# Optimization experiments

Hardware: AMD Instinct MI355X
Metric: run time of the kernel (lower is better)

Reference implementation:

```python
import jax, jax.numpy as jnp
import numpy as np

D_MODEL = 768
N_HEADS = 12
D_K = D_MODEL // N_HEADS
NEG_INF = -1e9


def setup_inputs() -> dict:
    key = jax.random.key(0)
    ks = jax.random.split(key, 7)
    B, S = 4, 2048
    x = jax.random.normal(ks[0], (B, S, D_MODEL), dtype=jnp.float32)
    # causal mask, broadcastable to [B, H, S, S]
    mask = jnp.tril(jnp.ones((S, S), dtype=bool))[None, None, :, :]
    scale = 1.0 / np.sqrt(D_MODEL)
    Wq = jax.random.normal(ks[1], (D_MODEL, D_MODEL), dtype=jnp.float32) * scale
    bq = jnp.zeros((D_MODEL,), dtype=jnp.float32)
    Wk = jax.random.normal(ks[2], (D_MODEL, D_MODEL), dtype=jnp.float32) * scale
    bk = jnp.zeros((D_MODEL,), dtype=jnp.float32)
    Wv = jax.random.normal(ks[3], (D_MODEL, D_MODEL), dtype=jnp.float32) * scale
    bv = jnp.zeros((D_MODEL,), dtype=jnp.float32)
    return {"x": x, "mask": mask, "Wq": Wq, "bq": bq, "Wk": Wk, "bk": bk, "Wv": Wv, "bv": bv}


def reference(x, mask, Wq, bq, Wk, bk, Wv, bv):
    B, S, _ = x.shape
    # projections (torch Linear: y = x @ W.T + b)
    q = (x @ Wq.T + bq).reshape(B, S, N_HEADS, D_K)
    k = (x @ Wk.T + bk).reshape(B, S, N_HEADS, D_K)
    v = (x @ Wv.T + bv).reshape(B, S, N_HEADS, D_K)
    # scores: [B, H, S, S]
    scores = jnp.einsum("bqhd,bkhd->bhqk", q, k) / jnp.sqrt(jnp.float32(D_K))
    scores = jnp.where(mask, scores, NEG_INF)
    probs = jax.nn.softmax(scores, axis=-1)
    # attention: [B, H, S, D_K] -> [B, S, d_model]
    attn = jnp.einsum("bhqk,bkhd->bqhd", probs, v).reshape(B, S, D_MODEL)
    return attn
```

## Files before the change

kernel.cpp:

```cpp
#include <hip/hip_runtime.h>
#include <math.h>


#define S_LEN 2048
#define BATCH 4
#define HEADS 12
#define DM 768
#define DK 64
#define BH (BATCH*HEADS)
#define MROWS (BATCH*S_LEN)
#define QSCALE 0.1803368801111244f

typedef __attribute__((ext_vector_type(8))) short short8;
typedef __attribute__((ext_vector_type(4))) float floatx4;
typedef __attribute__((address_space(3))) unsigned char lds_byte;
typedef __attribute__((address_space(1))) const unsigned char glob_byte;

__device__ __forceinline__ unsigned short f2bf(float f) {
  union { float f; unsigned int u; } a; a.f = f;
  unsigned int u = a.u;
  return (unsigned short)((u + 0x7fffu + ((u >> 16) & 1u)) >> 16);
}
__device__ __forceinline__ unsigned short f2bf_rtz(float f) {
  union { float f; unsigned int u; } a; a.f = f;
  return (unsigned short)(a.u >> 16);
}

__global__ void cast_f32_bf16(const float* __restrict__ src,
                              unsigned short* __restrict__ dst, int n) {
  int i = (blockIdx.x * blockDim.x + threadIdx.x) * 4;
  if (i < n) {
    float4 v = *(const float4*)(src + i);
    ushort4 o;
    o.x = f2bf(v.x); o.y = f2bf(v.y); o.z = f2bf(v.z); o.w = f2bf(v.w);
    *(ushort4*)(dst + i) = o;
  }
}

__global__ void cast_w3(const float* __restrict__ w0, const float* __restrict__ w1,
                        const float* __restrict__ w2, unsigned short* __restrict__ dst,
                        int n) {
  const float* src = (blockIdx.y == 0) ? w0 : (blockIdx.y == 1) ? w1 : w2;
  int i = (blockIdx.x * blockDim.x + threadIdx.x) * 4;
  if (i < n) {
    float4 v = *(const float4*)(src + i);
    ushort4 o;
    o.x = f2bf(v.x); o.y = f2bf(v.y); o.z = f2bf(v.z); o.w = f2bf(v.w);
    *(ushort4*)(dst + (size_t)blockIdx.y * n + i) = o;
  }
}

__global__ __launch_bounds__(256) void qkv_gemm(
    const unsigned short* __restrict__ xb,
    const unsigned short* __restrict__ wb,
    const float* __restrict__ bq, const float* __restrict__ bk,
    const float* __restrict__ bv,
    unsigned short* __restrict__ qo,
    unsigned short* __restrict__ ko,
    unsigned short* __restrict__ vto) {
  __shared__ unsigned short a_lds[2 * 128 * 32];
  __shared__ unsigned short b_lds[2 * 128 * 32];
  const int mat = blockIdx.z;
  const int tid = threadIdx.x;
  const int wave = tid >> 6, lane = tid & 63, quad = lane >> 4, ln = lane & 15;
  const int wm = wave & 1, wn = wave >> 1;
  const int m_blk = blockIdx.x * 128, n_blk = blockIdx.y * 128;
  const unsigned short* w = wb + (size_t)mat * DM * DM;
  const int srow_i[2] = { (0 * 256 + wave * 64 + lane) >> 2,
                          (1 * 256 + wave * 64 + lane) >> 2 };
  const int sq = (lane & 3) * 8;

  const floatx4 fz = {0.f, 0.f, 0.f, 0.f};
  floatx4 acc[4][4];
#pragma unroll
  for (int mg = 0; mg < 4; mg++)
#pragma unroll
    for (int c = 0; c < 4; c++) acc[mg][c] = fz;

  for (int k0 = 0; k0 < DM; k0 += 64) {
#pragma unroll
    for (int p = 0; p < 2; p++)
#pragma unroll
      for (int i = 0; i < 2; i++) {
        const int cbase = i * 256 + wave * 64;
        const int row = srow_i[i];
        __builtin_amdgcn_global_load_lds(
            (glob_byte*)(xb + (size_t)(m_blk + row) * DM + k0 + p * 32 + sq),
            (lds_byte*)(a_lds + p * 4096 + cbase * 8), 16, 0, 0);
        __builtin_amdgcn_global_load_lds(
            (glob_byte*)(w + (size_t)(n_blk + row) * DM + k0 + p * 32 + sq),
            (lds_byte*)(b_lds + p * 4096 + cbase * 8), 16, 0, 0);
      }
    __syncthreads();

    short8 af[4][2], bf[4][2];
#pragma unroll
    for (int mg = 0; mg < 4; mg++)
#pragma unroll
      for (int p = 0; p < 2; p++)
        af[mg][p] = *(const short8*)(a_lds + p * 4096 + (wm * 64 + mg * 16 + ln) * 32 + quad * 8);
#pragma unroll
    for (int c = 0; c < 4; c++)
#pragma unroll
      for (int p = 0; p < 2; p++)
        bf[c][p] = *(const short8*)(b_lds + p * 4096 + (wn * 64 + c * 16 + ln) * 32 + quad * 8);
#pragma unroll
    for (int mg = 0; mg < 4; mg++)
#pragma unroll
      for (int c = 0; c < 4; c++) {
        acc[mg][c] = __builtin_amdgcn_mfma_f32_16x16x32_bf16(af[mg][0], bf[c][0], acc[mg][c], 0, 0, 0);
        acc[mg][c] = __builtin_amdgcn_mfma_f32_16x16x32_bf16(af[mg][1], bf[c][1], acc[mg][c], 0, 0, 0);
      }
    __syncthreads();
  }

  const float* bias = (mat == 0) ? bq : (mat == 1) ? bk : bv;
  const float oscale = (mat == 0) ? QSCALE : 1.0f;
  const int m_base = m_blk + wm * 64, n_base = n_blk + wn * 64;
#pragma unroll
  for (int mg = 0; mg < 4; mg++)
#pragma unroll
    for (int c = 0; c < 4; c++) {
      int gn = n_base + c * 16 + ln;
      int hd = gn >> 6, d = gn & 63;
      float bias_v = bias[gn] * oscale;
      int gm0 = m_base + mg * 16 + quad * 4;
      int bb = gm0 >> 11, s0 = gm0 & (S_LEN - 1);
      if (mat == 2) {
        ushort4 pk;
        pk.x = f2bf(acc[mg][c][0] + bias_v);
        pk.y = f2bf(acc[mg][c][1] + bias_v);
        pk.z = f2bf(acc[mg][c][2] + bias_v);
        pk.w = f2bf(acc[mg][c][3] + bias_v);
        *(ushort4*)(vto + (((size_t)(bb * HEADS + hd)) * DK + d) * S_LEN + s0) = pk;
      } else {
        unsigned short* dst = (mat == 0 ? qo : ko) +
            (((size_t)(bb * HEADS + hd)) * S_LEN + s0) * DK + d;
#pragma unroll
        for (int r = 0; r < 4; r++)
          dst[(size_t)r * DK] = f2bf(acc[mg][c][r] * oscale + bias_v);
      }
    }
}

__global__ __launch_bounds__(128) void flash_attn(
    const unsigned short* __restrict__ q,
    const unsigned short* __restrict__ k,
    const unsigned short* __restrict__ vt,
    float* __restrict__ out) {
  __shared__ unsigned short p_lds[2][32 * 64];
  const int id = blockIdx.x;
  const int bh = id % BH;
  const int qt = (S_LEN / 64 - 1) - (id / BH);
  const int q0 = qt * 64;
  const int tid = threadIdx.x;
  const int wave = tid >> 6, lane = tid & 63, quad = lane >> 4, ln = lane & 15;
  unsigned short* pl = p_lds[wave];
  const unsigned short* qp = q  + (size_t)bh * S_LEN * DK;
  const unsigned short* kp = k  + (size_t)bh * S_LEN * DK;
  const unsigned short* vp = vt + (size_t)bh * DK * S_LEN;
  const int qr_base = q0 + wave * 32;
  const floatx4 fz = {0.f, 0.f, 0.f, 0.f};

  unsigned short* wp[4];
#pragma unroll
  for (int kg = 0; kg < 4; kg++)
    wp[kg] = pl + quad * 256 + (((((kg ^ quad) & 3) << 1) | (ln >> 3)) * 8) + (ln & 7);
  const unsigned short* rp[2];
#pragma unroll
  for (int ss = 0; ss < 2; ss++)
    rp[ss] = pl + ln * 64 + (((ss * 4 + quad) ^ (((ln >> 2) & 3) << 1)) * 8);

  const int klane = ln * DK + quad * 8;
  const int vlane = ln * S_LEN + quad * 8;

  short8 ones;
#pragma unroll
  for (int j = 0; j < 8; j++) ones[j] = (short)0x3F80;

  short8 aq[2][2];
#pragma unroll
  for (int h = 0; h < 2; h++)
#pragma unroll
    for (int ss = 0; ss < 2; ss++)
      aq[h][ss] = *(const short8*)(qp + (qr_base + h * 16 + ln) * DK + ss * 32 + quad * 8);

  floatx4 o[2][4];
  floatx4 ol[2] = {fz, fz};
#pragma unroll
  for (int h = 0; h < 2; h++) {
    o[h][0] = fz; o[h][1] = fz; o[h][2] = fz; o[h][3] = fz;
  }

  auto loadK = [&](int k0, short8 (&kf)[4][2]) {
#pragma unroll
    for (int kg = 0; kg < 4; kg++)
#pragma unroll
      for (int ss = 0; ss < 2; ss++)
        kf[kg][ss] = *(const short8*)(kp + klane + (k0 + kg * 16) * DK + ss * 32);
  };

  auto body = [&](int k0, short8 (&kf)[4][2]) {
    short8 vf[4][2];
#pragma unroll
    for (int dg = 0; dg < 4; dg++)
#pragma unroll
      for (int ss = 0; ss < 2; ss++)
        vf[dg][ss] = *(const short8*)(vp + vlane + dg * 16 * S_LEN + k0 + ss * 32);
    const bool domask = (k0 + 63 > qr_base);
#pragma unroll
    for (int h = 0; h < 2; h++) {
      floatx4 sc[4];
#pragma unroll
      for (int kg = 0; kg < 4; kg++) {
        floatx4 tt = __builtin_amdgcn_mfma_f32_16x16x32_bf16(aq[h][0], kf[kg][0], fz, 0, 0, 0);
        sc[kg] = __builtin_amdgcn_mfma_f32_16x16x32_bf16(aq[h][1], kf[kg][1], tt, 0, 0, 0);
      }
#pragma unroll
      for (int kg = 0; kg < 4; kg++) {
        int key = k0 + kg * 16 + ln;
#pragma unroll
        for (int r = 0; r < 4; r++) {
          float pv = exp2f(sc[kg][r]);
          if (domask) {
            int qr = qr_base + h * 16 + quad * 4 + r;
            pv = (key <= qr) ? pv : 0.f;
          }
          wp[kg][h * 1024 + r * 64] = f2bf_rtz(pv);
        }
      }
      short8 ap0 = *(const short8*)(rp[0] + h * 1024);
      short8 ap1 = *(const short8*)(rp[1] + h * 1024);
#pragma unroll
      for (int dg = 0; dg < 4; dg++) {
        o[h][dg] = __builtin_amdgcn_mfma_f32_16x16x32_bf16(ap0, vf[dg][0], o[h][dg], 0, 0, 0);
        o[h][dg] = __builtin_amdgcn_mfma_f32_16x16x32_bf16(ap1, vf[dg][1], o[h][dg], 0, 0, 0);
      }
      ol[h] = __builtin_amdgcn_mfma_f32_16x16x32_bf16(ap0, ones, ol[h], 0, 0, 0);
      ol[h] = __builtin_amdgcn_mfma_f32_16x16x32_bf16(ap1, ones, ol[h], 0, 0, 0);
    }
  };

  const int kend = qr_base + 32;
  short8 kfa[4][2], kfb[4][2];
  loadK(0, kfa);
  int k0 = 0;
  for (; k0 + 64 < kend; k0 += 128) {
    loadK(k0 + 64, kfb);
    body(k0, kfa);
    loadK(k0 + 128, kfa);
    body(k0 + 64, kfb);
  }
  if (k0 < kend) body(k0, kfa);

  const int b = bh / HEADS, hd = bh % HEADS;
#pragma unroll
  for (int h = 0; h < 2; h++)
#pragma unroll
    for (int r = 0; r < 4; r++) {
      float inv = 1.f / ol[h][r];
      int qr = qr_base + h * 16 + quad * 4 + r;
      float* orow = out + ((size_t)(b * S_LEN + qr)) * DM + hd * DK;
      orow[ln]      = o[h][0][r] * inv;
      orow[16 + ln] = o[h][1][r] * inv;
      orow[32 + ln] = o[h][2][r] * inv;
      orow[48 + ln] = o[h][3][r] * inv;
    }
}

extern "C" void kernel_launch(void* const* d_in, const int* in_sizes, int n_in,
                              void* d_out, int out_size, void* d_ws, size_t ws_size,
                              hipStream_t stream) {
  const float* x  = (const float*)d_in[0];
  const float* Wq = (const float*)d_in[2];
  const float* bq = (const float*)d_in[3];
  const float* Wk = (const float*)d_in[4];
  const float* bk = (const float*)d_in[5];
  const float* Wv = (const float*)d_in[6];
  const float* bv = (const float*)d_in[7];
  float* out = (float*)d_out;

  const int NX = MROWS * DM;
  const int NW = DM * DM;
  unsigned short* xb = (unsigned short*)d_ws;
  unsigned short* wb = xb + NX;
  unsigned short* qo = wb + 3 * NW;
  unsigned short* ko = qo + (size_t)BH * S_LEN * DK;
  unsigned short* vt = ko + (size_t)BH * S_LEN * DK;

  cast_f32_bf16<<<(NX / 4 + 255) / 256, 256, 0, stream>>>(x, xb, NX);
  cast_w3<<<dim3((NW / 4 + 255) / 256, 3), 256, 0, stream>>>(Wq, Wk, Wv, wb, NW);

  qkv_gemm<<<dim3(MROWS / 128, DM / 128, 3), 256, 0, stream>>>(
      xb, wb, bq, bk, bv, qo, ko, vt);

  flash_attn<<<dim3((S_LEN / 64) * BH), 128, 0, stream>>>(qo, ko, vt, out);
}
```

Before: 254.3 us.

## Keep attention probabilities in registers using 32x32 MFMA and permlane32 swaps

Rewrites the flash-attention inner loop to use 32x32x16 bf16 MFMAs. Scores are computed transposed, with K as the A operand. The probabilities are packed with v_cvt_pk_bf16_f32 and rearranged across lane halves with v_permlane32_swap, so they feed the P·V MFMA directly. This removes the shared-memory write/read round trip and its swizzle addressing for P, and cuts the MFMA instruction count. In exchange it relies on gfx950-specific instructions, changes P rounding from truncation to round-to-nearest, and uses larger 16-float accumulators that raise register pressure.

Result: no change. 256.1 us (+0.7%).

```diff
diff --git a/kernel.cpp b/kernel.cpp
--- a/kernel.cpp
+++ b/kernel.cpp
@@ -13,6 +13,8 @@
 
 typedef __attribute__((ext_vector_type(8))) short short8;
 typedef __attribute__((ext_vector_type(4))) float floatx4;
+typedef __attribute__((ext_vector_type(16))) float floatx16;
+typedef __attribute__((ext_vector_type(4))) unsigned int uintx4;
 typedef __attribute__((address_space(3))) unsigned char lds_byte;
 typedef __attribute__((address_space(1))) const unsigned char glob_byte;
 
@@ -20,10 +22,6 @@
   union { float f; unsigned int u; } a; a.f = f;
   unsigned int u = a.u;
   return (unsigned short)((u + 0x7fffu + ((u >> 16) & 1u)) >> 16);
-}
-__device__ __forceinline__ unsigned short f2bf_rtz(float f) {
-  union { float f; unsigned int u; } a; a.f = f;
-  return (unsigned short)(a.u >> 16);
 }
 
 __global__ void cast_f32_bf16(const float* __restrict__ src,
@@ -148,101 +146,92 @@
     const unsigned short* __restrict__ k,
     const unsigned short* __restrict__ vt,
     float* __restrict__ out) {
-  __shared__ unsigned short p_lds[2][32 * 64];
   const int id = blockIdx.x;
   const int bh = id % BH;
   const int qt = (S_LEN / 64 - 1) - (id / BH);
   const int q0 = qt * 64;
   const int tid = threadIdx.x;
-  const int wave = tid >> 6, lane = tid & 63, quad = lane >> 4, ln = lane & 15;
-  unsigned short* pl = p_lds[wave];
+  const int wave = tid >> 6, lane = tid & 63;
+  const int l31 = lane & 31, hi = lane >> 5;
   const unsigned short* qp = q  + (size_t)bh * S_LEN * DK;
   const unsigned short* kp = k  + (size_t)bh * S_LEN * DK;
   const unsigned short* vp = vt + (size_t)bh * DK * S_LEN;
   const int qr_base = q0 + wave * 32;
-  const floatx4 fz = {0.f, 0.f, 0.f, 0.f};
-
-  unsigned short* wp[4];
-#pragma unroll
-  for (int kg = 0; kg < 4; kg++)
-    wp[kg] = pl + quad * 256 + (((((kg ^ quad) & 3) << 1) | (ln >> 3)) * 8) + (ln & 7);
-  const unsigned short* rp[2];
-#pragma unroll
-  for (int ss = 0; ss < 2; ss++)
-    rp[ss] = pl + ln * 64 + (((ss * 4 + quad) ^ (((ln >> 2) & 3) << 1)) * 8);
-
-  const int klane = ln * DK + quad * 8;
-  const int vlane = ln * S_LEN + quad * 8;
+
+  const floatx16 fz16 = {0.f,0.f,0.f,0.f,0.f,0.f,0.f,0.f,
+                         0.f,0.f,0.f,0.f,0.f,0.f,0.f,0.f};
 
   short8 ones;
 #pragma unroll
   for (int j = 0; j < 8; j++) ones[j] = (short)0x3F80;
 
-  short8 aq[2][2];
-#pragma unroll
-  for (int h = 0; h < 2; h++)
-#pragma unroll
-    for (int ss = 0; ss < 2; ss++)
-      aq[h][ss] = *(const short8*)(qp + (qr_base + h * 16 + ln) * DK + ss * 32 + quad * 8);
-
-  floatx4 o[2][4];
-  floatx4 ol[2] = {fz, fz};
-#pragma unroll
-  for (int h = 0; h < 2; h++) {
-    o[h][0] = fz; o[h][1] = fz; o[h][2] = fz; o[h][3] = fz;
-  }
-
-  auto loadK = [&](int k0, short8 (&kf)[4][2]) {
-#pragma unroll
-    for (int kg = 0; kg < 4; kg++)
-#pragma unroll
-      for (int ss = 0; ss < 2; ss++)
-        kf[kg][ss] = *(const short8*)(kp + klane + (k0 + kg * 16) * DK + ss * 32);
+  short8 aq[4];
+#pragma unroll
+  for (int ks = 0; ks < 4; ks++)
+    aq[ks] = *(const short8*)(qp + (size_t)(qr_base + l31) * DK + ks * 16 + hi * 8);
+
+  floatx16 o0 = fz16, o1 = fz16, lacc = fz16;
+
+  auto loadK = [&](int k0, short8 (&kf)[2][4]) {
+#pragma unroll
+    for (int kg = 0; kg < 2; kg++)
+#pragma unroll
+      for (int ks = 0; ks < 4; ks++)
+        kf[kg][ks] = *(const short8*)(kp + (size_t)(k0 + kg * 32 + l31) * DK + ks * 16 + hi * 8);
   };
 
-  auto body = [&](int k0, short8 (&kf)[4][2]) {
-    short8 vf[4][2];
-#pragma unroll
-    for (int dg = 0; dg < 4; dg++)
-#pragma unroll
-      for (int ss = 0; ss < 2; ss++)
-        vf[dg][ss] = *(const short8*)(vp + vlane + dg * 16 * S_LEN + k0 + ss * 32);
+  auto body = [&](int k0, short8 (&kf)[2][4]) {
+    short8 vf[2][2][2];
+#pragma unroll
+    for (int dg = 0; dg < 2; dg++)
+#pragma unroll
+      for (int kg = 0; kg < 2; kg++)
+#pragma unroll
+        for (int ks2 = 0; ks2 < 2; ks2++)
+          vf[dg][kg][ks2] = *(const short8*)(vp + (size_t)(dg * 32 + l31) * S_LEN
+                                             + k0 + kg * 32 + ks2 * 16 + hi * 8);
     const bool domask = (k0 + 63 > qr_base);
 #pragma unroll
-    for (int h = 0; h < 2; h++) {
-      floatx4 sc[4];
-#pragma unroll
-      for (int kg = 0; kg < 4; kg++) {
-        floatx4 tt = __builtin_amdgcn_mfma_f32_16x16x32_bf16(aq[h][0], kf[kg][0], fz, 0, 0, 0);
-        sc[kg] = __builtin_amdgcn_mfma_f32_16x16x32_bf16(aq[h][1], kf[kg][1], tt, 0, 0, 0);
-      }
-#pragma unroll
-      for (int kg = 0; kg < 4; kg++) {
-        int key = k0 + kg * 16 + ln;
-#pragma unroll
-        for (int r = 0; r < 4; r++) {
-          float pv = exp2f(sc[kg][r]);
-          if (domask) {
-            int qr = qr_base + h * 16 + quad * 4 + r;
-            pv = (key <= qr) ? pv : 0.f;
-          }
-          wp[kg][h * 1024 + r * 64] = f2bf_rtz(pv);
+    for (int kg = 0; kg < 2; kg++) {
+      floatx16 sc = fz16;
+#pragma unroll
+      for (int ks = 0; ks < 4; ks++)
+        sc = __builtin_amdgcn_mfma_f32_32x32x16_bf16(kf[kg][ks], aq[ks], sc, 0, 0, 0);
+      float pv[16];
+      const int qr = qr_base + l31;
+#pragma unroll
+      for (int r = 0; r < 16; r++) {
+        float e = exp2f(sc[r]);
+        if (domask) {
+          int key = k0 + kg * 32 + (r & 3) + 8 * (r >> 2) + 4 * hi;
+          e = (key <= qr) ? e : 0.f;
         }
-      }
-      short8 ap0 = *(const short8*)(rp[0] + h * 1024);
-      short8 ap1 = *(const short8*)(rp[1] + h * 1024);
-#pragma unroll
-      for (int dg = 0; dg < 4; dg++) {
-        o[h][dg] = __builtin_amdgcn_mfma_f32_16x16x32_bf16(ap0, vf[dg][0], o[h][dg], 0, 0, 0);
-        o[h][dg] = __builtin_amdgcn_mfma_f32_16x16x32_bf16(ap1, vf[dg][1], o[h][dg], 0, 0, 0);
-      }
-      ol[h] = __builtin_amdgcn_mfma_f32_16x16x32_bf16(ap0, ones, ol[h], 0, 0, 0);
-      ol[h] = __builtin_amdgcn_mfma_f32_16x16x32_bf16(ap1, ones, ol[h], 0, 0, 0);
+        pv[r] = e;
+      }
+      unsigned int dw[4][2];
+#pragma unroll
+      for (int b = 0; b < 4; b++)
+#pragma unroll
+        for (int c = 0; c < 2; c++)
+          asm("v_cvt_pk_bf16_f32 %0, %1, %2"
+              : "=v"(dw[b][c]) : "v"(pv[4 * b + 2 * c]), "v"(pv[4 * b + 2 * c + 1]));
+#pragma unroll
+      for (int ks2 = 0; ks2 < 2; ks2++) {
+        unsigned int a0 = dw[2 * ks2][0], a1 = dw[2 * ks2][1];
+        unsigned int b0 = dw[2 * ks2 + 1][0], b1 = dw[2 * ks2 + 1][1];
+        asm("v_permlane32_swap_b32 %0, %1" : "+v"(a0), "+v"(b0));
+        asm("v_permlane32_swap_b32 %0, %1" : "+v"(a1), "+v"(b1));
+        union { uintx4 u; short8 s; } ap;
+        ap.u = (uintx4){a0, a1, b0, b1};
+        o0 = __builtin_amdgcn_mfma_f32_32x32x16_bf16(ap.s, vf[0][kg][ks2], o0, 0, 0, 0);
+        o1 = __builtin_amdgcn_mfma_f32_32x32x16_bf16(ap.s, vf[1][kg][ks2], o1, 0, 0, 0);
+        lacc = __builtin_amdgcn_mfma_f32_32x32x16_bf16(ap.s, ones, lacc, 0, 0, 0);
+      }
     }
   };
 
   const int kend = qr_base + 32;
-  short8 kfa[4][2], kfb[4][2];
+  short8 kfa[2][4], kfb[2][4];
   loadK(0, kfa);
   int k0 = 0;
   for (; k0 + 64 < kend; k0 += 128) {
@@ -255,17 +244,13 @@
 
   const int b = bh / HEADS, hd = bh % HEADS;
 #pragma unroll
-  for (int h = 0; h < 2; h++)
-#pragma unroll
-    for (int r = 0; r < 4; r++) {
-      float inv = 1.f / ol[h][r];
-      int qr = qr_base + h * 16 + quad * 4 + r;
-      float* orow = out + ((size_t)(b * S_LEN + qr)) * DM + hd * DK;
-      orow[ln]      = o[h][0][r] * inv;
-      orow[16 + ln] = o[h][1][r] * inv;
-      orow[32 + ln] = o[h][2][r] * inv;
-      orow[48 + ln] = o[h][3][r] * inv;
-    }
+  for (int r = 0; r < 16; r++) {
+    float inv = 1.f / lacc[r];
+    int qrow = qr_base + (r & 3) + 8 * (r >> 2) + 4 * hi;
+    float* orow = out + ((size_t)(b * S_LEN + qrow)) * DM + hd * DK;
+    orow[l31]      = o0[r] * inv;
+    orow[32 + l31] = o1[r] * inv;
+  }
 }
 
 extern "C" void kernel_launch(void* const* d_in, const int* in_sizes, int n_in,
```
